# Kernel optimization log

Hardware: AMD Instinct MI355X
Metric: run time of the kernel (lower is better)

Reference implementation:

```python
import jax, jax.numpy as jnp
import numpy as np


def _cas(N, dtype=jnp.float32):
    # cas(2*pi*k*n/N) = cos + sin, symmetric NxN matrix (rebuilt per call, as in the original)
    n = jnp.arange(N, dtype=dtype)
    ang = (2.0 * jnp.pi / N) * jnp.outer(n, n)
    return jnp.cos(ang) + jnp.sin(ang)


def dht(x):
    # Discrete Hartley transform over the last axis via dense matmul
    return x @ _cas(x.shape[-1], x.dtype)


def reverse(x):
    # X[(N - k) mod N]: index 0 stays, rest are flipped
    return jnp.roll(jnp.flip(x, axis=-1), 1, axis=-1)


def setup_inputs() -> dict:
    key = jax.random.key(0)
    k1, k2 = jax.random.split(key)
    B, Cin, Cout, N, M = 4, 16, 16, 8192, 64
    x = jax.random.normal(k1, (B, Cin, N), dtype=jnp.float32)
    scale = 1.0 / (Cin * Cout)
    weights1 = scale * jax.random.uniform(k2, (Cin, Cout, M), dtype=jnp.float32)
    return {"x": x, "weights1": weights1}


def reference(x, weights1):
    B, Cin, N = x.shape
    Cout, M = weights1.shape[1], weights1.shape[2]
    N2 = N // 2 + 1

    # DHT of the input over the spatial axis
    x_ht = dht(x)                                   # [B, Cin, N]

    # compl_mul1d on the first `modes1` Hartley coefficients
    hp = dht(x_ht[:, :, :M])                        # [B, Cin, M] (DHT applied again, as in source)
    hq = dht(weights1)                              # [Cin, Cout, M]
    rp = reverse(hp)
    rq = reverse(hq)
    # (t1 + t2 + t3 - t4)/2 == ((hp+rp)@hq + (hp-rp)@rq)/2
    hz = 0.5 * (jnp.einsum('bix,iox->box', hp + rp, hq)
                + jnp.einsum('bix,iox->box', hp - rp, rq))  # [B, Cout, M]
    # idht normalizes by the TOTAL element count of its argument (quirk preserved)
    z = dht(hz) / (B * Cout * M)                    # [B, Cout, M]

    # Scatter into half-spectrum buffer, then idht (imag part is always zero -> stay real)
    out_ht = jnp.zeros((B, Cout, N2), dtype=x.dtype).at[:, :, :M].set(z)
    out = dht(out_ht) / (B * Cout * N2)             # [B, Cout, N//2 + 1]
    return out
```

## Files before the change

### kernel.cpp

```cpp
#include <hip/hip_runtime.h>
#include <math.h>

#define TWO_PI 6.283185307179586f

__global__ __launch_bounds__(256) void kA(const float* __restrict__ x,
                                          const float* __restrict__ w1,
                                          float* __restrict__ P,
                                          float* __restrict__ hq) {
  __shared__ float sH[128], cH[128], sL[64], cL[64];
  __shared__ float rows[4][64];
  __shared__ float cas64[64];
  const int blk = blockIdx.x;
  const int t = threadIdx.x;

  if (blk < 256) {
    if (t < 128) {
      float s, c;
      __sincosf((float)t * (TWO_PI / 128.0f), &s, &c);
      sH[t] = s;
      cH[t] = c;
    } else if (t < 192) {
      const int g = t - 128;
      float s, c;
      __sincosf((float)g * (TWO_PI / 8192.0f), &s, &c);
      sL[g] = s;
      cL[g] = c;
    }
    __syncthreads();

    const int r  = blk & 63;
    const int mb = (blk >> 6) & 1;
    const int nh = (blk >> 7) & 1;
    const int l  = t & 63;
    const int w  = t >> 6;
    const int mbase = mb * 32 + w * 8;
    const float* xr = x + r * 8192 + nh * 4096;

    float u[8], v[8], Cs[8], Ss[8];
    float accA[8][4];
    float accB[8][3];

#pragma unroll
    for (int q = 0; q < 8; ++q) {
      const int m = mbase + q;
      const int idx0 = ((nh * 4096 + 4 * l) * m) & 8191;
      const int h = idx0 >> 6, g = idx0 & 63;
      const float c0 = cH[h] * cL[g] - sH[h] * sL[g];
      const float s0 = sH[h] * cL[g] + cH[h] * sL[g];
      u[q] = c0 + s0;
      v[q] = c0 - s0;
      const int ih = (4 * m) & 127;
      Cs[q] = cH[ih];
      Ss[q] = sH[ih];
#pragma unroll
      for (int j = 0; j < 4; ++j) accA[q][j] = 0.0f;
#pragma unroll
      for (int j = 0; j < 3; ++j) accB[q][j] = 0.0f;
    }

#pragma unroll 8
    for (int it = 0; it < 16; ++it) {
      const float4 xv = *reinterpret_cast<const float4*>(xr + it * 256 + 4 * l);
#pragma unroll
      for (int q = 0; q < 8; ++q) {
        accA[q][0] += xv.x * u[q];
        accA[q][1] += xv.y * u[q];
        accA[q][2] += xv.z * u[q];
        accA[q][3] += xv.w * u[q];
        accB[q][0] += xv.y * v[q];
        accB[q][1] += xv.z * v[q];
        accB[q][2] += xv.w * v[q];
        const float un = Cs[q] * u[q] + Ss[q] * v[q];
        const float vn = Cs[q] * v[q] - Ss[q] * u[q];
        u[q] = un;
        v[q] = vn;
      }
    }

    float cval, sval;
    {
      const int qq = (l >> 2) & 7;
      const int jj = l & 3;
      const int jm = jj * (mbase + qq);
      const int h = jm >> 6, g = jm & 63;
      cval = cH[h] * cL[g] - sH[h] * sL[g];
      sval = sH[h] * cL[g] + cH[h] * sL[g];
    }

#pragma unroll
    for (int q = 0; q < 8; ++q) {
      float acc = accA[q][0];
#pragma unroll
      for (int j = 1; j < 4; ++j) {
        const float cj = __shfl(cval, q * 4 + j, 64);
        const float sj = __shfl(sval, q * 4 + j, 64);
        acc += cj * accA[q][j] + sj * accB[q][j - 1];
      }
#pragma unroll
      for (int off = 32; off > 0; off >>= 1) acc += __shfl_xor(acc, off, 64);
      if (l == q) P[(r * 64 + (mbase + q)) * 2 + nh] = acc;
    }
  } else {
    const int sub = t >> 6;
    const int c = t & 63;
    if (t < 64) {
      float s, cc;
      __sincosf((float)t * (TWO_PI / 64.0f), &s, &cc);
      cas64[t] = cc + s;
    }
    const int b2 = blk - 256;
    rows[sub][c] = w1[(b2 * 4 + sub) * 64 + c];
    __syncthreads();
    float acc = 0.0f;
#pragma unroll 8
    for (int m = 0; m < 64; ++m) acc += rows[sub][m] * cas64[(m * c) & 63];
    hq[(b2 * 4 + sub) * 64 + c] = acc;
  }
}

__global__ __launch_bounds__(256) void kB(const float* __restrict__ P,
                                          const float* __restrict__ hq,
                                          float* __restrict__ z) {
  const int blk = blockIdx.x;
  const int b = blk >> 4;
  const int o = blk & 15;
  __shared__ float sAT[64][20];
  __shared__ float sq[16][64];
  __shared__ float hp[16][64];
  __shared__ float hz[64];
  __shared__ float red[4][64];
  __shared__ float cas64[64];
  const int t = threadIdx.x;
  const int m = t & 63;
  const int sub = t >> 6;

  if (t < 64) {
    float s, cc;
    __sincosf((float)t * (TWO_PI / 64.0f), &s, &cc);
    cas64[t] = cc + s;
  }
  for (int idx = t; idx < 1024; idx += 256) {
    const int i = idx >> 6;
    const int c = idx & 63;
    const float2 pv =
        *reinterpret_cast<const float2*>(&P[(((b * 16 + i) << 6) + c) * 2]);
    sAT[c][i] = pv.x + pv.y;
    sq[i][c] = hq[(((i * 16 + o) << 6)) + c];
  }
  __syncthreads();

  {
    float sd, cd;
    __sincosf((float)m * (TWO_PI / 64.0f), &sd, &cd);
    float u = 1.0f, v = 1.0f;
    float acc0 = 0.0f, acc1 = 0.0f, acc2 = 0.0f, acc3 = 0.0f;
#pragma unroll 8
    for (int c = 0; c < 64; ++c) {
      const float4 av = *reinterpret_cast<const float4*>(&sAT[c][sub * 4]);
      acc0 += av.x * u;
      acc1 += av.y * u;
      acc2 += av.z * u;
      acc3 += av.w * u;
      const float un = cd * u + sd * v;
      const float vn = cd * v - sd * u;
      u = un;
      v = vn;
    }
    hp[sub * 4 + 0][m] = acc0;
    hp[sub * 4 + 1][m] = acc1;
    hp[sub * 4 + 2][m] = acc2;
    hp[sub * 4 + 3][m] = acc3;
  }
  __syncthreads();

  const int mr = (64 - m) & 63;
  float a = 0.0f;
#pragma unroll
  for (int ii = 0; ii < 4; ++ii) {
    const int i = sub * 4 + ii;
    const float p  = hp[i][m];
    const float pr = hp[i][mr];
    const float qq = sq[i][m];
    const float qr = sq[i][mr];
    a += 0.5f * ((p + pr) * qq + (p - pr) * qr);
  }
  red[sub][m] = a;
  __syncthreads();
  if (t < 64) hz[t] = red[0][t] + red[1][t] + red[2][t] + red[3][t];
  __syncthreads();

  float zz = 0.0f;
#pragma unroll
  for (int jj = 0; jj < 16; ++jj) {
    const int mm = sub * 16 + jj;
    zz += hz[mm] * cas64[(mm * m) & 63];
  }
  red[sub][m] = zz;
  __syncthreads();
  if (t < 64)
    z[blk * 64 + t] =
        (red[0][t] + red[1][t] + red[2][t] + red[3][t]) * (1.0f / 4096.0f);
}

__global__ __launch_bounds__(256) void kC(const float* __restrict__ z,
                                          float* __restrict__ out) {
  const int row = blockIdx.x;
  const int kc  = blockIdx.y;
  __shared__ float zr[64];
  const int t = threadIdx.x;
  if (t < 64) zr[t] = z[row * 64 + t];
  __syncthreads();
  const int k = kc * 256 + t;
  if (k >= 4097) return;
  const float th = (float)k * (TWO_PI / 4097.0f);
  float s1, c1;
  __sincosf(th, &s1, &c1);

  float cw[8], sw[8];
  cw[0] = 1.0f; sw[0] = 0.0f;
  cw[1] = c1;   sw[1] = s1;
#pragma unroll
  for (int b = 2; b < 8; ++b) {
    cw[b] = cw[b - 1] * c1 - sw[b - 1] * s1;
    sw[b] = sw[b - 1] * c1 + cw[b - 1] * s1;
  }
  const float c8 = cw[7] * c1 - sw[7] * s1;
  const float s8 = sw[7] * c1 + cw[7] * s1;

  float A[8], B[8];
#pragma unroll
  for (int b = 0; b < 8; ++b) { A[b] = 0.0f; B[b] = 0.0f; }
  float u = 1.0f, v = 1.0f;
#pragma unroll
  for (int a = 0; a < 8; ++a) {
#pragma unroll
    for (int b = 0; b < 8; ++b) {
      const float zz = zr[a * 8 + b];
      A[b] += zz * u;
      B[b] += zz * v;
    }
    const float un = c8 * u + s8 * v;
    const float vn = c8 * v - s8 * u;
    u = un;
    v = vn;
  }
  float acc = 0.0f;
#pragma unroll
  for (int b = 0; b < 8; ++b) acc += cw[b] * A[b] + sw[b] * B[b];
  out[row * 4097 + k] = acc * (1.0f / 262208.0f);
}

extern "C" void kernel_launch(void* const* d_in, const int* in_sizes, int n_in,
                              void* d_out, int out_size, void* d_ws, size_t ws_size,
                              hipStream_t stream) {
  const float* x  = (const float*)d_in[0];
  const float* w1 = (const float*)d_in[1];
  float* out = (float*)d_out;
  float* ws = (float*)d_ws;
  float* P  = ws;
  float* hq = ws + 8192;
  float* z  = ws + 24576;

  kA<<<320, 256, 0, stream>>>(x, w1, P, hq);
  kB<<<64, 256, 0, stream>>>(P, hq, z);
  kC<<<dim3(64, 17), 256, 0, stream>>>(z, out);
}
```

Measured before the change: 72.19 us.

## Replace DHT-multiply-IDHT chain with direct circular convolution in kB

Uses the Hartley convolution theorem so that the DHT of hp, the Hartley-domain product with hq, and the inverse DHT collapse into a direct circular convolution of the summed P rows with the raw weights. This removes the hq computation from kA, along with the DHT and inverse-DHT loops and several barriers in kB. kB is also split across 256 blocks, each computing a 16-mode slice, to raise parallelism. The risk is numerical: the 1/64 scaling and the index conventions must match the original algebra exactly.

```diff
diff --git a/kernel.cpp b/kernel.cpp
--- a/kernel.cpp
+++ b/kernel.cpp
@@ -4,202 +4,149 @@
 #define TWO_PI 6.283185307179586f
 
 __global__ __launch_bounds__(256) void kA(const float* __restrict__ x,
-                                          const float* __restrict__ w1,
-                                          float* __restrict__ P,
-                                          float* __restrict__ hq) {
+                                          float* __restrict__ P) {
   __shared__ float sH[128], cH[128], sL[64], cL[64];
-  __shared__ float rows[4][64];
-  __shared__ float cas64[64];
   const int blk = blockIdx.x;
   const int t = threadIdx.x;
 
-  if (blk < 256) {
-    if (t < 128) {
-      float s, c;
-      __sincosf((float)t * (TWO_PI / 128.0f), &s, &c);
-      sH[t] = s;
-      cH[t] = c;
-    } else if (t < 192) {
-      const int g = t - 128;
-      float s, c;
-      __sincosf((float)g * (TWO_PI / 8192.0f), &s, &c);
-      sL[g] = s;
-      cL[g] = c;
-    }
-    __syncthreads();
-
-    const int r  = blk & 63;
-    const int mb = (blk >> 6) & 1;
-    const int nh = (blk >> 7) & 1;
-    const int l  = t & 63;
-    const int w  = t >> 6;
-    const int mbase = mb * 32 + w * 8;
-    const float* xr = x + r * 8192 + nh * 4096;
-
-    float u[8], v[8], Cs[8], Ss[8];
-    float accA[8][4];
-    float accB[8][3];
-
+  if (t < 128) {
+    float s, c;
+    __sincosf((float)t * (TWO_PI / 128.0f), &s, &c);
+    sH[t] = s;
+    cH[t] = c;
+  } else if (t < 192) {
+    const int g = t - 128;
+    float s, c;
+    __sincosf((float)g * (TWO_PI / 8192.0f), &s, &c);
+    sL[g] = s;
+    cL[g] = c;
+  }
+  __syncthreads();
+
+  const int r  = blk & 63;
+  const int mb = (blk >> 6) & 1;
+  const int nh = (blk >> 7) & 1;
+  const int l  = t & 63;
+  const int w  = t >> 6;
+  const int mbase = mb * 32 + w * 8;
+  const float* xr = x + r * 8192 + nh * 4096;
+
+  float u[8], v[8], Cs[8], Ss[8];
+  float accA[8][4];
+  float accB[8][3];
+
+#pragma unroll
+  for (int q = 0; q < 8; ++q) {
+    const int m = mbase + q;
+    const int idx0 = ((nh * 4096 + 4 * l) * m) & 8191;
+    const int h = idx0 >> 6, g = idx0 & 63;
+    const float c0 = cH[h] * cL[g] - sH[h] * sL[g];
+    const float s0 = sH[h] * cL[g] + cH[h] * sL[g];
+    u[q] = c0 + s0;
+    v[q] = c0 - s0;
+    const int ih = (4 * m) & 127;
+    Cs[q] = cH[ih];
+    Ss[q] = sH[ih];
+#pragma unroll
+    for (int j = 0; j < 4; ++j) accA[q][j] = 0.0f;
+#pragma unroll
+    for (int j = 0; j < 3; ++j) accB[q][j] = 0.0f;
+  }
+
+#pragma unroll 8
+  for (int it = 0; it < 16; ++it) {
+    const float4 xv = *reinterpret_cast<const float4*>(xr + it * 256 + 4 * l);
 #pragma unroll
     for (int q = 0; q < 8; ++q) {
-      const int m = mbase + q;
-      const int idx0 = ((nh * 4096 + 4 * l) * m) & 8191;
-      const int h = idx0 >> 6, g = idx0 & 63;
-      const float c0 = cH[h] * cL[g] - sH[h] * sL[g];
-      const float s0 = sH[h] * cL[g] + cH[h] * sL[g];
-      u[q] = c0 + s0;
-      v[q] = c0 - s0;
-      const int ih = (4 * m) & 127;
-      Cs[q] = cH[ih];
-      Ss[q] = sH[ih];
-#pragma unroll
-      for (int j = 0; j < 4; ++j) accA[q][j] = 0.0f;
-#pragma unroll
-      for (int j = 0; j < 3; ++j) accB[q][j] = 0.0f;
-    }
-
-#pragma unroll 8
-    for (int it = 0; it < 16; ++it) {
-      const float4 xv = *reinterpret_cast<const float4*>(xr + it * 256 + 4 * l);
-#pragma unroll
-      for (int q = 0; q < 8; ++q) {
-        accA[q][0] += xv.x * u[q];
-        accA[q][1] += xv.y * u[q];
-        accA[q][2] += xv.z * u[q];
-        accA[q][3] += xv.w * u[q];
-        accB[q][0] += xv.y * v[q];
-        accB[q][1] += xv.z * v[q];
-        accB[q][2] += xv.w * v[q];
-        const float un = Cs[q] * u[q] + Ss[q] * v[q];
-        const float vn = Cs[q] * v[q] - Ss[q] * u[q];
-        u[q] = un;
-        v[q] = vn;
-      }
-    }
-
-    float cval, sval;
-    {
-      const int qq = (l >> 2) & 7;
-      const int jj = l & 3;
-      const int jm = jj * (mbase + qq);
-      const int h = jm >> 6, g = jm & 63;
-      cval = cH[h] * cL[g] - sH[h] * sL[g];
-      sval = sH[h] * cL[g] + cH[h] * sL[g];
-    }
-
-#pragma unroll
-    for (int q = 0; q < 8; ++q) {
-      float acc = accA[q][0];
-#pragma unroll
-      for (int j = 1; j < 4; ++j) {
-        const float cj = __shfl(cval, q * 4 + j, 64);
-        const float sj = __shfl(sval, q * 4 + j, 64);
-        acc += cj * accA[q][j] + sj * accB[q][j - 1];
-      }
-#pragma unroll
-      for (int off = 32; off > 0; off >>= 1) acc += __shfl_xor(acc, off, 64);
-      if (l == q) P[(r * 64 + (mbase + q)) * 2 + nh] = acc;
-    }
-  } else {
-    const int sub = t >> 6;
-    const int c = t & 63;
-    if (t < 64) {
-      float s, cc;
-      __sincosf((float)t * (TWO_PI / 64.0f), &s, &cc);
-      cas64[t] = cc + s;
-    }
-    const int b2 = blk - 256;
-    rows[sub][c] = w1[(b2 * 4 + sub) * 64 + c];
-    __syncthreads();
-    float acc = 0.0f;
-#pragma unroll 8
-    for (int m = 0; m < 64; ++m) acc += rows[sub][m] * cas64[(m * c) & 63];
-    hq[(b2 * 4 + sub) * 64 + c] = acc;
+      accA[q][0] += xv.x * u[q];
+      accA[q][1] += xv.y * u[q];
+      accA[q][2] += xv.z * u[q];
+      accA[q][3] += xv.w * u[q];
+      accB[q][0] += xv.y * v[q];
+      accB[q][1] += xv.z * v[q];
+      accB[q][2] += xv.w * v[q];
+      const float un = Cs[q] * u[q] + Ss[q] * v[q];
+      const float vn = Cs[q] * v[q] - Ss[q] * u[q];
+      u[q] = un;
+      v[q] = vn;
+    }
+  }
+
+  float cval, sval;
+  {
+    const int qq = (l >> 2) & 7;
+    const int jj = l & 3;
+    const int jm = jj * (mbase + qq);
+    const int h = jm >> 6, g = jm & 63;
+    cval = cH[h] * cL[g] - sH[h] * sL[g];
+    sval = sH[h] * cL[g] + cH[h] * sL[g];
+  }
+
+#pragma unroll
+  for (int q = 0; q < 8; ++q) {
+    float acc = accA[q][0];
+#pragma unroll
+    for (int j = 1; j < 4; ++j) {
+      const float cj = __shfl(cval, q * 4 + j, 64);
+      const float sj = __shfl(sval, q * 4 + j, 64);
+      acc += cj * accA[q][j] + sj * accB[q][j - 1];
+    }
+#pragma unroll
+    for (int off = 32; off > 0; off >>= 1) acc += __shfl_xor(acc, off, 64);
+    if (l == q) P[(r * 64 + (mbase + q)) * 2 + nh] = acc;
   }
 }
 
 __global__ __launch_bounds__(256) void kB(const float* __restrict__ P,
-                                          const float* __restrict__ hq,
+                                          const float* __restrict__ w1,
                                           float* __restrict__ z) {
   const int blk = blockIdx.x;
-  const int b = blk >> 4;
-  const int o = blk & 15;
-  __shared__ float sAT[64][20];
-  __shared__ float sq[16][64];
-  __shared__ float hp[16][64];
-  __shared__ float hz[64];
-  __shared__ float red[4][64];
-  __shared__ float cas64[64];
+  const int b  = blk >> 6;
+  const int o  = (blk >> 2) & 15;
+  const int mq = blk & 3;
+  __shared__ float sA[16][64];
+  __shared__ float sW[16][64];
+  __shared__ float red[4][16];
   const int t = threadIdx.x;
-  const int m = t & 63;
-  const int sub = t >> 6;
-
-  if (t < 64) {
-    float s, cc;
-    __sincosf((float)t * (TWO_PI / 64.0f), &s, &cc);
-    cas64[t] = cc + s;
-  }
+
   for (int idx = t; idx < 1024; idx += 256) {
     const int i = idx >> 6;
     const int c = idx & 63;
     const float2 pv =
         *reinterpret_cast<const float2*>(&P[(((b * 16 + i) << 6) + c) * 2]);
-    sAT[c][i] = pv.x + pv.y;
-    sq[i][c] = hq[(((i * 16 + o) << 6)) + c];
-  }
-  __syncthreads();
-
-  {
-    float sd, cd;
-    __sincosf((float)m * (TWO_PI / 64.0f), &sd, &cd);
-    float u = 1.0f, v = 1.0f;
-    float acc0 = 0.0f, acc1 = 0.0f, acc2 = 0.0f, acc3 = 0.0f;
-#pragma unroll 8
-    for (int c = 0; c < 64; ++c) {
-      const float4 av = *reinterpret_cast<const float4*>(&sAT[c][sub * 4]);
-      acc0 += av.x * u;
-      acc1 += av.y * u;
-      acc2 += av.z * u;
-      acc3 += av.w * u;
-      const float un = cd * u + sd * v;
-      const float vn = cd * v - sd * u;
-      u = un;
-      v = vn;
-    }
-    hp[sub * 4 + 0][m] = acc0;
-    hp[sub * 4 + 1][m] = acc1;
-    hp[sub * 4 + 2][m] = acc2;
-    hp[sub * 4 + 3][m] = acc3;
-  }
-  __syncthreads();
-
-  const int mr = (64 - m) & 63;
-  float a = 0.0f;
+    sA[i][c] = pv.x + pv.y;
+    sW[i][c] = w1[((i * 16 + o) << 6) + c];
+  }
+  __syncthreads();
+
+  const int w  = t >> 6;
+  const int l  = t & 63;
+  const int jq = l >> 4;
+  const int ml = l & 15;
+  const int m  = mq * 16 + ml;
+
+  float acc = 0.0f;
 #pragma unroll
   for (int ii = 0; ii < 4; ++ii) {
-    const int i = sub * 4 + ii;
-    const float p  = hp[i][m];
-    const float pr = hp[i][mr];
-    const float qq = sq[i][m];
-    const float qr = sq[i][mr];
-    a += 0.5f * ((p + pr) * qq + (p - pr) * qr);
-  }
-  red[sub][m] = a;
-  __syncthreads();
-  if (t < 64) hz[t] = red[0][t] + red[1][t] + red[2][t] + red[3][t];
-  __syncthreads();
-
-  float zz = 0.0f;
-#pragma unroll
-  for (int jj = 0; jj < 16; ++jj) {
-    const int mm = sub * 16 + jj;
-    zz += hz[mm] * cas64[(mm * m) & 63];
-  }
-  red[sub][m] = zz;
-  __syncthreads();
-  if (t < 64)
-    z[blk * 64 + t] =
-        (red[0][t] + red[1][t] + red[2][t] + red[3][t]) * (1.0f / 4096.0f);
+    const int i = w * 4 + ii;
+#pragma unroll
+    for (int jb = 0; jb < 4; ++jb) {
+      const float4 a4 =
+          *reinterpret_cast<const float4*>(&sA[i][jq * 16 + jb * 4]);
+      const int j0 = jq * 16 + jb * 4;
+      acc += a4.x * sW[i][(m - j0) & 63];
+      acc += a4.y * sW[i][(m - j0 - 1) & 63];
+      acc += a4.z * sW[i][(m - j0 - 2) & 63];
+      acc += a4.w * sW[i][(m - j0 - 3) & 63];
+    }
+  }
+  acc += __shfl_xor(acc, 16, 64);
+  acc += __shfl_xor(acc, 32, 64);
+  if (jq == 0) red[w][ml] = acc;
+  __syncthreads();
+  if (t < 16)
+    z[(((b * 16 + o) << 6)) + m] =
+        (red[0][t] + red[1][t] + red[2][t] + red[3][t]) * (1.0f / 64.0f);
 }
 
 __global__ __launch_bounds__(256) void kC(const float* __restrict__ z,
@@ -258,10 +205,9 @@
   float* out = (float*)d_out;
   float* ws = (float*)d_ws;
   float* P  = ws;
-  float* hq = ws + 8192;
-  float* z  = ws + 24576;
-
-  kA<<<320, 256, 0, stream>>>(x, w1, P, hq);
-  kB<<<64, 256, 0, stream>>>(P, hq, z);
+  float* z  = ws + 8192;
+
+  kA<<<256, 256, 0, stream>>>(x, P);
+  kB<<<256, 256, 0, stream>>>(P, w1, z);
   kC<<<dim3(64, 17), 256, 0, stream>>>(z, out);
 }
```

Measured after the change: 70.36 us. 2.5% less time.
